# Optimization experiments

Measured on AMD Instinct MI355X. Metric: run time of the kernel, lower is better.

Reference implementation:

```python
import jax, jax.numpy as jnp
import numpy as np

SEQ = 4096
D = 1024


def setup_inputs() -> dict:
    key = jax.random.key(0)
    kx, kq, kk, kv = jax.random.split(key, 4)
    x = jax.random.normal(kx, (SEQ, D), dtype=jnp.float32)
    W_Q = jax.random.normal(kq, (D, D), dtype=jnp.float32)
    W_K = jax.random.normal(kk, (D, D), dtype=jnp.float32)
    W_V = jax.random.normal(kv, (D, D), dtype=jnp.float32)
    b_Q = jnp.zeros((D,), dtype=jnp.float32)
    b_K = jnp.zeros((D,), dtype=jnp.float32)
    b_V = jnp.zeros((D,), dtype=jnp.float32)
    return {"x": x, "W_Q": W_Q, "W_K": W_K, "W_V": W_V,
            "b_Q": b_Q, "b_K": b_K, "b_V": b_V}


def reference(x, W_Q, W_K, W_V, b_Q, b_K, b_V):
    d_head = W_Q.shape[0]
    q = x @ W_Q + b_Q                      # [S, D]
    k = x @ W_K + b_K                      # [S, D]
    v = x @ W_V + b_V                      # [S, D]
    scores = (q @ k.T) / jnp.sqrt(jnp.float32(d_head))  # [S, S]
    probs = jax.nn.softmax(scores, axis=-1)              # softmax over last axis
    return probs @ v                        # [S, D]
```

## Files before the change

kernel.cpp:

```cpp
#include <hip/hip_runtime.h>
#include <hip/hip_bf16.h>
#include <stdint.h>

#define SEQLEN 4096
#define DMODEL 1024

typedef uint16_t u16;
typedef uint32_t u32;

typedef __bf16 bf16x8 __attribute__((ext_vector_type(8)));
typedef float  f32x4  __attribute__((ext_vector_type(4)));
typedef u16    u16x8  __attribute__((ext_vector_type(8)));
typedef u16    u16x4  __attribute__((ext_vector_type(4)));

__device__ __forceinline__ u16 f2bf(float f) {
  union { float f; u32 u; } a; a.f = f;
  return (u16)((a.u + 0x7FFFu + ((a.u >> 16) & 1u)) >> 16);
}
__device__ __forceinline__ float bf2f(u16 h) {
  union { u32 u; float f; } a; a.u = ((u32)h) << 16;
  return a.f;
}

__device__ __forceinline__ void gl_lds16(const u16* g, u16* l) {
  __builtin_amdgcn_global_load_lds(
      (const __attribute__((address_space(1))) void*)g,
      (__attribute__((address_space(3))) void*)l,
      16, 0, 0);
}

__device__ __forceinline__ void stage_tile(const u16* __restrict__ g, int ld,
                                           int row0, int k0, u16* lds, int tid) {
#pragma unroll
  for (int it = 0; it < 4; ++it) {
    int u = tid + 256 * it;
    int row = u >> 3;
    int cg = (u & 7) ^ (row & 7);
    gl_lds16(g + (size_t)(row0 + row) * ld + (size_t)(k0 + cg * 8), lds + u * 8);
  }
}

__device__ __forceinline__ bf16x8 ld_frag(const u16* lds, int row, int chunk) {
  return *(const bf16x8*)(lds + row * 64 + ((chunk ^ (row & 7)) << 3));
}

#define MFMA16(c, a, b) c = __builtin_amdgcn_mfma_f32_16x16x32_bf16(a, b, c, 0, 0, 0)

__global__ void split_x_kernel(const float* __restrict__ x,
                               u16* __restrict__ xh, u16* __restrict__ xl) {
  const int total = SEQLEN * DMODEL / 4;
  for (int idx = blockIdx.x * 256 + threadIdx.x; idx < total; idx += gridDim.x * 256) {
    float4 f = ((const float4*)x)[idx];
    float ff[4] = {f.x, f.y, f.z, f.w};
    union { u16x4 v; u16 s[4]; } h, l;
#pragma unroll
    for (int uu = 0; uu < 4; ++uu) {
      u16 hi = f2bf(ff[uu]);
      h.s[uu] = hi;
      l.s[uu] = f2bf(ff[uu] - bf2f(hi));
    }
    ((u16x4*)xh)[idx] = h.v;
    ((u16x4*)xl)[idx] = l.v;
  }
}

__global__ void transpose_w_kernel(const float* __restrict__ W,
                                   u16* __restrict__ wth, u16* __restrict__ wtl) {
  __shared__ float tile[64][65];
  int n0 = (blockIdx.x & 15) * 64;
  int k0 = (blockIdx.x >> 4) * 64;
  int c = threadIdx.x & 63, r0 = threadIdx.x >> 6;
#pragma unroll
  for (int rr = 0; rr < 16; ++rr) {
    int r = r0 * 16 + rr;
    tile[r][c] = W[(size_t)(k0 + r) * DMODEL + n0 + c];
  }
  __syncthreads();
#pragma unroll
  for (int rr = 0; rr < 16; ++rr) {
    int n = r0 * 16 + rr;
    float f = tile[c][n];
    u16 hi = f2bf(f);
    wth[(size_t)(n0 + n) * DMODEL + k0 + c] = hi;
    wtl[(size_t)(n0 + n) * DMODEL + k0 + c] = f2bf(f - bf2f(hi));
  }
}

template <bool THREE, bool SPLITOUT>
__global__ __launch_bounds__(256, 2) void proj_kernel(
    const u16* __restrict__ Ah, const u16* __restrict__ Al,
    const u16* __restrict__ Bh, const u16* __restrict__ Bl,
    const float* __restrict__ bias, float scale,
    u16* __restrict__ outh, u16* __restrict__ outl, u16* __restrict__ outT) {
  __shared__ __align__(16) u16 sAh[128 * 64];
  __shared__ __align__(16) u16 sBh[128 * 64];
  __shared__ __align__(16) u16 sAl[THREE ? 128 * 64 : 8];
  __shared__ __align__(16) u16 sBl[THREE ? 128 * 64 : 8];

  int tid = threadIdx.x;
  int lane = tid & 63, wid = tid >> 6;
  int wr = (wid >> 1) * 64, wc = (wid & 1) * 64;
  int r = lane & 15, g = lane >> 4;
  int m0 = blockIdx.x * 128, n0 = blockIdx.y * 128;

  f32x4 acc[4][4];
#pragma unroll
  for (int i = 0; i < 4; ++i)
#pragma unroll
    for (int j = 0; j < 4; ++j) acc[i][j] = (f32x4){0.f, 0.f, 0.f, 0.f};

  for (int step = 0; step < DMODEL / 64; ++step) {
    int k0 = step * 64;
    __syncthreads();
    stage_tile(Ah, DMODEL, m0, k0, sAh, tid);
    stage_tile(Bh, DMODEL, n0, k0, sBh, tid);
    if (THREE) {
      stage_tile(Al, DMODEL, m0, k0, sAl, tid);
      stage_tile(Bl, DMODEL, n0, k0, sBl, tid);
    }
    __syncthreads();
#pragma unroll
    for (int ks = 0; ks < 2; ++ks) {
      bf16x8 fa[4], fb[4], fal[4], fbl[4];
#pragma unroll
      for (int i = 0; i < 4; ++i) {
        fa[i] = ld_frag(sAh, wr + i * 16 + r, ks * 4 + g);
        fb[i] = ld_frag(sBh, wc + i * 16 + r, ks * 4 + g);
      }
      if (THREE) {
#pragma unroll
        for (int i = 0; i < 4; ++i) {
          fal[i] = ld_frag(sAl, wr + i * 16 + r, ks * 4 + g);
          fbl[i] = ld_frag(sBl, wc + i * 16 + r, ks * 4 + g);
        }
      }
#pragma unroll
      for (int i = 0; i < 4; ++i)
#pragma unroll
        for (int j = 0; j < 4; ++j) {
          MFMA16(acc[i][j], fa[i], fb[j]);
          if (THREE) {
            MFMA16(acc[i][j], fa[i], fbl[j]);
            MFMA16(acc[i][j], fal[i], fb[j]);
          }
        }
    }
  }
#pragma unroll
  for (int i = 0; i < 4; ++i)
#pragma unroll
    for (int j = 0; j < 4; ++j) {
      int col = n0 + wc + j * 16 + r;
      float bv = bias[col];
#pragma unroll
      for (int t = 0; t < 4; ++t) {
        int row = m0 + wr + i * 16 + g * 4 + t;
        float v = (acc[i][j][t] + bv) * scale;
        if (SPLITOUT) {
          u16 hi = f2bf(v);
          outh[(size_t)row * DMODEL + col] = hi;
          outl[(size_t)row * DMODEL + col] = f2bf(v - bf2f(hi));
        } else {
          outT[(size_t)col * SEQLEN + row] = f2bf(v);
        }
      }
    }
}

__global__ __launch_bounds__(256, 2) void scores_kernel(
    const u16* __restrict__ qh, const u16* __restrict__ ql,
    const u16* __restrict__ kh, const u16* __restrict__ kl,
    u16* __restrict__ P, float* __restrict__ mloc, float* __restrict__ tsum) {
  __shared__ __align__(16) float sS[128 * 129];
  u16* sAh = (u16*)sS;
  u16* sAl = sAh + 128 * 64;
  u16* sBh = sAl + 128 * 64;
  u16* sBl = sBh + 128 * 64;

  int tid = threadIdx.x;
  int lane = tid & 63, wid = tid >> 6;
  int wr = (wid >> 1) * 64, wc = (wid & 1) * 64;
  int r = lane & 15, g = lane >> 4;
  int m0 = blockIdx.x * 128, n0 = blockIdx.y * 128;

  f32x4 acc[4][4];
#pragma unroll
  for (int i = 0; i < 4; ++i)
#pragma unroll
    for (int j = 0; j < 4; ++j) acc[i][j] = (f32x4){0.f, 0.f, 0.f, 0.f};

  for (int step = 0; step < DMODEL / 64; ++step) {
    int k0 = step * 64;
    __syncthreads();
    stage_tile(qh, DMODEL, m0, k0, sAh, tid);
    stage_tile(kh, DMODEL, n0, k0, sBh, tid);
    stage_tile(ql, DMODEL, m0, k0, sAl, tid);
    stage_tile(kl, DMODEL, n0, k0, sBl, tid);
    __syncthreads();
#pragma unroll
    for (int ks = 0; ks < 2; ++ks) {
      bf16x8 fa[4], fb[4], fal[4], fbl[4];
#pragma unroll
      for (int i = 0; i < 4; ++i) {
        fa[i] = ld_frag(sAh, wr + i * 16 + r, ks * 4 + g);
        fb[i] = ld_frag(sBh, wc + i * 16 + r, ks * 4 + g);
        fal[i] = ld_frag(sAl, wr + i * 16 + r, ks * 4 + g);
        fbl[i] = ld_frag(sBl, wc + i * 16 + r, ks * 4 + g);
      }
#pragma unroll
      for (int i = 0; i < 4; ++i)
#pragma unroll
        for (int j = 0; j < 4; ++j) {
          MFMA16(acc[i][j], fa[i], fb[j]);
          MFMA16(acc[i][j], fa[i], fbl[j]);
          MFMA16(acc[i][j], fal[i], fb[j]);
        }
    }
  }
  __syncthreads();
#pragma unroll
  for (int i = 0; i < 4; ++i)
#pragma unroll
    for (int j = 0; j < 4; ++j)
#pragma unroll
      for (int t = 0; t < 4; ++t)
        sS[(wr + i * 16 + g * 4 + t) * 129 + wc + j * 16 + r] = acc[i][j][t];
  __syncthreads();

  int rt = tid >> 1, h = tid & 1;
  const float* rowp = sS + rt * 129 + h * 64;
  float mx = -3.0e38f;
#pragma unroll 16
  for (int c = 0; c < 64; ++c) mx = fmaxf(mx, rowp[c]);
  mx = fmaxf(mx, __shfl_xor(mx, 1));

  float ssum = 0.f;
  int grow = m0 + rt;
  u16* pout = P + (size_t)grow * SEQLEN + n0 + h * 64;
#pragma unroll
  for (int c8 = 0; c8 < 8; ++c8) {
    union { u16 s[8]; u16x8 v; } tmp;
#pragma unroll
    for (int uu = 0; uu < 8; ++uu) {
      float e = exp2f((rowp[c8 * 8 + uu] - mx) * 1.4426950408889634f);
      ssum += e;
      tmp.s[uu] = f2bf(e);
    }
    *(u16x8*)(pout + c8 * 8) = tmp.v;
  }
  ssum += __shfl_xor(ssum, 1);
  if (h == 0) {
    mloc[(size_t)blockIdx.y * SEQLEN + grow] = mx;
    tsum[(size_t)blockIdx.y * SEQLEN + grow] = ssum;
  }
}

__global__ void finalize_kernel(const float* __restrict__ mloc,
                                const float* __restrict__ tsum,
                                float* __restrict__ rowscale) {
  int rr = blockIdx.x * 256 + threadIdx.x;
  if (rr >= SEQLEN) return;
  float M = -3.0e38f;
#pragma unroll
  for (int t = 0; t < 32; ++t) M = fmaxf(M, mloc[t * SEQLEN + rr]);
  float l = 0.f;
#pragma unroll
  for (int t = 0; t < 32; ++t)
    l += tsum[t * SEQLEN + rr] * exp2f((mloc[t * SEQLEN + rr] - M) * 1.4426950408889634f);
  float inv = 1.0f / l;
#pragma unroll
  for (int t = 0; t < 32; ++t)
    rowscale[t * SEQLEN + rr] = exp2f((mloc[t * SEQLEN + rr] - M) * 1.4426950408889634f) * inv;
}

__global__ void pnorm_kernel(u16* __restrict__ P, const float* __restrict__ rowscale) {
  const int total = SEQLEN * SEQLEN / 8;
  for (int idx = blockIdx.x * 256 + threadIdx.x; idx < total; idx += gridDim.x * 256) {
    int rrow = idx >> 9;
    int c8 = idx & 511;
    int t = c8 >> 4;
    float sc = rowscale[t * SEQLEN + rrow];
    union { u16x8 v; u16 s[8]; } d;
    d.v = ((u16x8*)P)[idx];
#pragma unroll
    for (int uu = 0; uu < 8; ++uu) d.s[uu] = f2bf(bf2f(d.s[uu]) * sc);
    ((u16x8*)P)[idx] = d.v;
  }
}

__global__ __launch_bounds__(256, 2) void pv_kernel(const u16* __restrict__ P,
                                                    const u16* __restrict__ vT,
                                                    float* __restrict__ out) {
  __shared__ __align__(16) u16 sA[128 * 64];
  __shared__ __align__(16) u16 sB[128 * 64];
  int tid = threadIdx.x;
  int lane = tid & 63, wid = tid >> 6;
  int wr = (wid >> 1) * 64, wc = (wid & 1) * 64;
  int r = lane & 15, g = lane >> 4;
  int m0 = blockIdx.x * 128, n0 = blockIdx.y * 128;

  f32x4 acc[4][4];
#pragma unroll
  for (int i = 0; i < 4; ++i)
#pragma unroll
    for (int j = 0; j < 4; ++j) acc[i][j] = (f32x4){0.f, 0.f, 0.f, 0.f};

  for (int step = 0; step < SEQLEN / 64; ++step) {
    int k0 = step * 64;
    __syncthreads();
    stage_tile(P, SEQLEN, m0, k0, sA, tid);
    stage_tile(vT, SEQLEN, n0, k0, sB, tid);
    __syncthreads();
#pragma unroll
    for (int ks = 0; ks < 2; ++ks) {
      bf16x8 fa[4], fb[4];
#pragma unroll
      for (int i = 0; i < 4; ++i) {
        fa[i] = ld_frag(sA, wr + i * 16 + r, ks * 4 + g);
        fb[i] = ld_frag(sB, wc + i * 16 + r, ks * 4 + g);
      }
#pragma unroll
      for (int i = 0; i < 4; ++i)
#pragma unroll
        for (int j = 0; j < 4; ++j) MFMA16(acc[i][j], fa[i], fb[j]);
    }
  }
#pragma unroll
  for (int i = 0; i < 4; ++i)
#pragma unroll
    for (int j = 0; j < 4; ++j)
#pragma unroll
      for (int t = 0; t < 4; ++t)
        out[(size_t)(m0 + wr + i * 16 + g * 4 + t) * DMODEL + n0 + wc + j * 16 + r] =
            acc[i][j][t];
}

extern "C" void kernel_launch(void* const* d_in, const int* in_sizes, int n_in,
                              void* d_out, int out_size, void* d_ws, size_t ws_size,
                              hipStream_t stream) {
  (void)in_sizes; (void)n_in; (void)out_size; (void)ws_size;
  const float* x  = (const float*)d_in[0];
  const float* WQ = (const float*)d_in[1];
  const float* WK = (const float*)d_in[2];
  const float* WV = (const float*)d_in[3];
  const float* bQ = (const float*)d_in[4];
  const float* bK = (const float*)d_in[5];
  const float* bV = (const float*)d_in[6];
  float* out = (float*)d_out;
  char* ws = (char*)d_ws;
  const size_t MB = 1ull << 20;

  u16* xh   = (u16*)(ws + 0);
  u16* xl   = (u16*)(ws + 8 * MB);
  u16* wqh  = (u16*)(ws + 16 * MB);
  u16* wql  = (u16*)(ws + 18 * MB);
  u16* wkh  = (u16*)(ws + 20 * MB);
  u16* wkl  = (u16*)(ws + 22 * MB);
  u16* wvh  = (u16*)(ws + 24 * MB);
  u16* wvl  = (u16*)(ws + 26 * MB);
  u16* P    = (u16*)(ws + 0);
  u16* qh   = (u16*)(ws + 32 * MB);
  u16* ql   = (u16*)(ws + 40 * MB);
  u16* kh   = (u16*)(ws + 48 * MB);
  u16* kl   = (u16*)(ws + 56 * MB);
  u16* vT   = (u16*)(ws + 64 * MB);
  float* mloc     = (float*)(ws + 72 * MB);
  float* tsum     = (float*)(ws + 72 * MB + 512 * 1024);
  float* rowscale = (float*)(ws + 73 * MB);

  split_x_kernel<<<2048, 256, 0, stream>>>(x, xh, xl);
  transpose_w_kernel<<<256, 256, 0, stream>>>(WQ, wqh, wql);
  transpose_w_kernel<<<256, 256, 0, stream>>>(WK, wkh, wkl);
  transpose_w_kernel<<<256, 256, 0, stream>>>(WV, wvh, wvl);

  dim3 gproj(32, 8);
  proj_kernel<true, true><<<gproj, 256, 0, stream>>>(xh, xl, wqh, wql, bQ,
                                                     1.0f / 32.0f, qh, ql, nullptr);
  proj_kernel<true, true><<<gproj, 256, 0, stream>>>(xh, xl, wkh, wkl, bK,
                                                     1.0f, kh, kl, nullptr);
  proj_kernel<false, false><<<gproj, 256, 0, stream>>>(xh, nullptr, wvh, nullptr, bV,
                                                       1.0f, nullptr, nullptr, vT);

  dim3 gsc(32, 32);
  scores_kernel<<<gsc, 256, 0, stream>>>(qh, ql, kh, kl, P, mloc, tsum);
  finalize_kernel<<<16, 256, 0, stream>>>(mloc, tsum, rowscale);
  pnorm_kernel<<<4096, 256, 0, stream>>>(P, rowscale);

  dim3 gpv(32, 8);
  pv_kernel<<<gpv, 256, 0, stream>>>(P, vT, out);
}
```

Baseline: 341.4 us.

## Fuse prep kernels, fold row scaling into PV, shrink LDS tiles, register softmax

Merges the x-split and three weight-transpose kernels into one launch. Removes the separate P normalization pass by applying per-tile row scales inside the PV GEMM. The three-term GEMMs now use 32-wide K tiles so LDS drops to 32KB and launch bounds allow more blocks per CU. The scores softmax works directly on accumulator registers with shuffles instead of spilling the score tile to LDS. In exchange there are twice as many K-loop barriers, extra scaling work in PV, and P is stored as scattered 2-byte writes.

```diff
diff --git a/kernel.cpp b/kernel.cpp
--- a/kernel.cpp
+++ b/kernel.cpp
@@ -29,8 +29,8 @@
       16, 0, 0);
 }
 
-__device__ __forceinline__ void stage_tile(const u16* __restrict__ g, int ld,
-                                           int row0, int k0, u16* lds, int tid) {
+__device__ __forceinline__ void stage64(const u16* __restrict__ g, int ld,
+                                        int row0, int k0, u16* lds, int tid) {
 #pragma unroll
   for (int it = 0; it < 4; ++it) {
     int u = tid + 256 * it;
@@ -39,63 +39,83 @@
     gl_lds16(g + (size_t)(row0 + row) * ld + (size_t)(k0 + cg * 8), lds + u * 8);
   }
 }
-
-__device__ __forceinline__ bf16x8 ld_frag(const u16* lds, int row, int chunk) {
+__device__ __forceinline__ void stage32(const u16* __restrict__ g, int ld,
+                                        int row0, int k0, u16* lds, int tid) {
+#pragma unroll
+  for (int it = 0; it < 2; ++it) {
+    int u = tid + 256 * it;
+    int row = u >> 2;
+    int cg = (u & 3) ^ ((row >> 1) & 3);
+    gl_lds16(g + (size_t)(row0 + row) * ld + (size_t)(k0 + cg * 8), lds + u * 8);
+  }
+}
+__device__ __forceinline__ bf16x8 frag64(const u16* lds, int row, int chunk) {
   return *(const bf16x8*)(lds + row * 64 + ((chunk ^ (row & 7)) << 3));
 }
+__device__ __forceinline__ bf16x8 frag32(const u16* lds, int row, int chunk) {
+  return *(const bf16x8*)(lds + row * 32 + ((chunk ^ ((row >> 1) & 3)) << 3));
+}
 
 #define MFMA16(c, a, b) c = __builtin_amdgcn_mfma_f32_16x16x32_bf16(a, b, c, 0, 0, 0)
 
-__global__ void split_x_kernel(const float* __restrict__ x,
-                               u16* __restrict__ xh, u16* __restrict__ xl) {
-  const int total = SEQLEN * DMODEL / 4;
-  for (int idx = blockIdx.x * 256 + threadIdx.x; idx < total; idx += gridDim.x * 256) {
-    float4 f = ((const float4*)x)[idx];
-    float ff[4] = {f.x, f.y, f.z, f.w};
-    union { u16x4 v; u16 s[4]; } h, l;
-#pragma unroll
-    for (int uu = 0; uu < 4; ++uu) {
-      u16 hi = f2bf(ff[uu]);
-      h.s[uu] = hi;
-      l.s[uu] = f2bf(ff[uu] - bf2f(hi));
-    }
-    ((u16x4*)xh)[idx] = h.v;
-    ((u16x4*)xl)[idx] = l.v;
-  }
-}
-
-__global__ void transpose_w_kernel(const float* __restrict__ W,
-                                   u16* __restrict__ wth, u16* __restrict__ wtl) {
+__global__ void prep_kernel(const float* __restrict__ x,
+                            const float* __restrict__ WQ,
+                            const float* __restrict__ WK,
+                            const float* __restrict__ WV,
+                            u16* __restrict__ xh, u16* __restrict__ xl,
+                            u16* __restrict__ wqh, u16* __restrict__ wql,
+                            u16* __restrict__ wkh, u16* __restrict__ wkl,
+                            u16* __restrict__ wvh, u16* __restrict__ wvl) {
   __shared__ float tile[64][65];
-  int n0 = (blockIdx.x & 15) * 64;
-  int k0 = (blockIdx.x >> 4) * 64;
-  int c = threadIdx.x & 63, r0 = threadIdx.x >> 6;
-#pragma unroll
-  for (int rr = 0; rr < 16; ++rr) {
-    int r = r0 * 16 + rr;
-    tile[r][c] = W[(size_t)(k0 + r) * DMODEL + n0 + c];
-  }
-  __syncthreads();
-#pragma unroll
-  for (int rr = 0; rr < 16; ++rr) {
-    int n = r0 * 16 + rr;
-    float f = tile[c][n];
-    u16 hi = f2bf(f);
-    wth[(size_t)(n0 + n) * DMODEL + k0 + c] = hi;
-    wtl[(size_t)(n0 + n) * DMODEL + k0 + c] = f2bf(f - bf2f(hi));
+  int bx = blockIdx.x;
+  if (bx < 768) {
+    const float* W = (bx < 256) ? WQ : (bx < 512) ? WK : WV;
+    u16* wth = (bx < 256) ? wqh : (bx < 512) ? wkh : wvh;
+    u16* wtl = (bx < 256) ? wql : (bx < 512) ? wkl : wvl;
+    int b = bx & 255;
+    int n0 = (b & 15) * 64;
+    int k0 = (b >> 4) * 64;
+    int c = threadIdx.x & 63, r0 = threadIdx.x >> 6;
+#pragma unroll
+    for (int rr = 0; rr < 16; ++rr) {
+      int r = r0 * 16 + rr;
+      tile[r][c] = W[(size_t)(k0 + r) * DMODEL + n0 + c];
+    }
+    __syncthreads();
+#pragma unroll
+    for (int rr = 0; rr < 16; ++rr) {
+      int n = r0 * 16 + rr;
+      float f = tile[c][n];
+      u16 hi = f2bf(f);
+      wth[(size_t)(n0 + n) * DMODEL + k0 + c] = hi;
+      wtl[(size_t)(n0 + n) * DMODEL + k0 + c] = f2bf(f - bf2f(hi));
+    }
+  } else {
+    const int total = SEQLEN * DMODEL / 4;
+    for (int idx = (bx - 768) * 256 + threadIdx.x; idx < total;
+         idx += (gridDim.x - 768) * 256) {
+      float4 f = ((const float4*)x)[idx];
+      float ff[4] = {f.x, f.y, f.z, f.w};
+      union { u16x4 v; u16 s[4]; } h, l;
+#pragma unroll
+      for (int uu = 0; uu < 4; ++uu) {
+        u16 hi = f2bf(ff[uu]);
+        h.s[uu] = hi;
+        l.s[uu] = f2bf(ff[uu] - bf2f(hi));
+      }
+      ((u16x4*)xh)[idx] = h.v;
+      ((u16x4*)xl)[idx] = l.v;
+    }
   }
 }
 
 template <bool THREE, bool SPLITOUT>
-__global__ __launch_bounds__(256, 2) void proj_kernel(
+__global__ __launch_bounds__(256, 4) void proj_kernel(
     const u16* __restrict__ Ah, const u16* __restrict__ Al,
     const u16* __restrict__ Bh, const u16* __restrict__ Bl,
     const float* __restrict__ bias, float scale,
     u16* __restrict__ outh, u16* __restrict__ outl, u16* __restrict__ outT) {
-  __shared__ __align__(16) u16 sAh[128 * 64];
-  __shared__ __align__(16) u16 sBh[128 * 64];
-  __shared__ __align__(16) u16 sAl[THREE ? 128 * 64 : 8];
-  __shared__ __align__(16) u16 sBl[THREE ? 128 * 64 : 8];
+  __shared__ __align__(16) u16 st[16384];
 
   int tid = threadIdx.x;
   int lane = tid & 63, wid = tid >> 6;
@@ -109,43 +129,55 @@
 #pragma unroll
     for (int j = 0; j < 4; ++j) acc[i][j] = (f32x4){0.f, 0.f, 0.f, 0.f};
 
-  for (int step = 0; step < DMODEL / 64; ++step) {
-    int k0 = step * 64;
-    __syncthreads();
-    stage_tile(Ah, DMODEL, m0, k0, sAh, tid);
-    stage_tile(Bh, DMODEL, n0, k0, sBh, tid);
-    if (THREE) {
-      stage_tile(Al, DMODEL, m0, k0, sAl, tid);
-      stage_tile(Bl, DMODEL, n0, k0, sBl, tid);
-    }
-    __syncthreads();
-#pragma unroll
-    for (int ks = 0; ks < 2; ++ks) {
+  if (THREE) {
+    for (int t = 0; t < DMODEL / 32; ++t) {
+      int k0 = t * 32;
+      __syncthreads();
+      stage32(Ah, DMODEL, m0, k0, st + 0 * 4096, tid);
+      stage32(Al, DMODEL, m0, k0, st + 1 * 4096, tid);
+      stage32(Bh, DMODEL, n0, k0, st + 2 * 4096, tid);
+      stage32(Bl, DMODEL, n0, k0, st + 3 * 4096, tid);
+      __syncthreads();
       bf16x8 fa[4], fb[4], fal[4], fbl[4];
 #pragma unroll
       for (int i = 0; i < 4; ++i) {
-        fa[i] = ld_frag(sAh, wr + i * 16 + r, ks * 4 + g);
-        fb[i] = ld_frag(sBh, wc + i * 16 + r, ks * 4 + g);
-      }
-      if (THREE) {
-#pragma unroll
-        for (int i = 0; i < 4; ++i) {
-          fal[i] = ld_frag(sAl, wr + i * 16 + r, ks * 4 + g);
-          fbl[i] = ld_frag(sBl, wc + i * 16 + r, ks * 4 + g);
-        }
+        fa[i]  = frag32(st + 0 * 4096, wr + i * 16 + r, g);
+        fal[i] = frag32(st + 1 * 4096, wr + i * 16 + r, g);
+        fb[i]  = frag32(st + 2 * 4096, wc + i * 16 + r, g);
+        fbl[i] = frag32(st + 3 * 4096, wc + i * 16 + r, g);
       }
 #pragma unroll
       for (int i = 0; i < 4; ++i)
 #pragma unroll
         for (int j = 0; j < 4; ++j) {
           MFMA16(acc[i][j], fa[i], fb[j]);
-          if (THREE) {
-            MFMA16(acc[i][j], fa[i], fbl[j]);
-            MFMA16(acc[i][j], fal[i], fb[j]);
-          }
+          MFMA16(acc[i][j], fa[i], fbl[j]);
+          MFMA16(acc[i][j], fal[i], fb[j]);
         }
     }
-  }
+  } else {
+    for (int t = 0; t < DMODEL / 64; ++t) {
+      int k0 = t * 64;
+      __syncthreads();
+      stage64(Ah, DMODEL, m0, k0, st + 0 * 8192, tid);
+      stage64(Bh, DMODEL, n0, k0, st + 1 * 8192, tid);
+      __syncthreads();
+#pragma unroll
+      for (int ks = 0; ks < 2; ++ks) {
+        bf16x8 fa[4], fb[4];
+#pragma unroll
+        for (int i = 0; i < 4; ++i) {
+          fa[i] = frag64(st + 0 * 8192, wr + i * 16 + r, ks * 4 + g);
+          fb[i] = frag64(st + 1 * 8192, wc + i * 16 + r, ks * 4 + g);
+        }
+#pragma unroll
+        for (int i = 0; i < 4; ++i)
+#pragma unroll
+          for (int j = 0; j < 4; ++j) MFMA16(acc[i][j], fa[i], fb[j]);
+      }
+    }
+  }
+
 #pragma unroll
   for (int i = 0; i < 4; ++i)
 #pragma unroll
@@ -167,20 +199,19 @@
     }
 }
 
-__global__ __launch_bounds__(256, 2) void scores_kernel(
+__global__ __launch_bounds__(256, 4) void scores_kernel(
     const u16* __restrict__ qh, const u16* __restrict__ ql,
     const u16* __restrict__ kh, const u16* __restrict__ kl,
     u16* __restrict__ P, float* __restrict__ mloc, float* __restrict__ tsum) {
-  __shared__ __align__(16) float sS[128 * 129];
-  u16* sAh = (u16*)sS;
-  u16* sAl = sAh + 128 * 64;
-  u16* sBh = sAl + 128 * 64;
-  u16* sBl = sBh + 128 * 64;
+  __shared__ __align__(16) u16 st[16384];
+  float* sm_max = (float*)st;
+  float* sm_sum = (float*)st + 256;
 
   int tid = threadIdx.x;
   int lane = tid & 63, wid = tid >> 6;
   int wr = (wid >> 1) * 64, wc = (wid & 1) * 64;
   int r = lane & 15, g = lane >> 4;
+  int halfid = wid & 1;
   int m0 = blockIdx.x * 128, n0 = blockIdx.y * 128;
 
   f32x4 acc[4][4];
@@ -189,69 +220,81 @@
 #pragma unroll
     for (int j = 0; j < 4; ++j) acc[i][j] = (f32x4){0.f, 0.f, 0.f, 0.f};
 
-  for (int step = 0; step < DMODEL / 64; ++step) {
-    int k0 = step * 64;
+  for (int t = 0; t < DMODEL / 32; ++t) {
+    int k0 = t * 32;
     __syncthreads();
-    stage_tile(qh, DMODEL, m0, k0, sAh, tid);
-    stage_tile(kh, DMODEL, n0, k0, sBh, tid);
-    stage_tile(ql, DMODEL, m0, k0, sAl, tid);
-    stage_tile(kl, DMODEL, n0, k0, sBl, tid);
+    stage32(qh, DMODEL, m0, k0, st + 0 * 4096, tid);
+    stage32(ql, DMODEL, m0, k0, st + 1 * 4096, tid);
+    stage32(kh, DMODEL, n0, k0, st + 2 * 4096, tid);
+    stage32(kl, DMODEL, n0, k0, st + 3 * 4096, tid);
     __syncthreads();
-#pragma unroll
-    for (int ks = 0; ks < 2; ++ks) {
-      bf16x8 fa[4], fb[4], fal[4], fbl[4];
-#pragma unroll
-      for (int i = 0; i < 4; ++i) {
-        fa[i] = ld_frag(sAh, wr + i * 16 + r, ks * 4 + g);
-        fb[i] = ld_frag(sBh, wc + i * 16 + r, ks * 4 + g);
-        fal[i] = ld_frag(sAl, wr + i * 16 + r, ks * 4 + g);
-        fbl[i] = ld_frag(sBl, wc + i * 16 + r, ks * 4 + g);
-      }
-#pragma unroll
-      for (int i = 0; i < 4; ++i)
-#pragma unroll
-        for (int j = 0; j < 4; ++j) {
-          MFMA16(acc[i][j], fa[i], fb[j]);
-          MFMA16(acc[i][j], fa[i], fbl[j]);
-          MFMA16(acc[i][j], fal[i], fb[j]);
-        }
-    }
-  }
+    bf16x8 fa[4], fb[4], fal[4], fbl[4];
+#pragma unroll
+    for (int i = 0; i < 4; ++i) {
+      fa[i]  = frag32(st + 0 * 4096, wr + i * 16 + r, g);
+      fal[i] = frag32(st + 1 * 4096, wr + i * 16 + r, g);
+      fb[i]  = frag32(st + 2 * 4096, wc + i * 16 + r, g);
+      fbl[i] = frag32(st + 3 * 4096, wc + i * 16 + r, g);
+    }
+#pragma unroll
+    for (int i = 0; i < 4; ++i)
+#pragma unroll
+      for (int j = 0; j < 4; ++j) {
+        MFMA16(acc[i][j], fa[i], fb[j]);
+        MFMA16(acc[i][j], fa[i], fbl[j]);
+        MFMA16(acc[i][j], fal[i], fb[j]);
+      }
+  }
+
   __syncthreads();
-#pragma unroll
-  for (int i = 0; i < 4; ++i)
-#pragma unroll
-    for (int j = 0; j < 4; ++j)
-#pragma unroll
-      for (int t = 0; t < 4; ++t)
-        sS[(wr + i * 16 + g * 4 + t) * 129 + wc + j * 16 + r] = acc[i][j][t];
+
+#pragma unroll
+  for (int i = 0; i < 4; ++i)
+#pragma unroll
+    for (int t = 0; t < 4; ++t) {
+      float m = fmaxf(fmaxf(acc[i][0][t], acc[i][1][t]),
+                      fmaxf(acc[i][2][t], acc[i][3][t]));
+      m = fmaxf(m, __shfl_xor(m, 1));
+      m = fmaxf(m, __shfl_xor(m, 2));
+      m = fmaxf(m, __shfl_xor(m, 4));
+      m = fmaxf(m, __shfl_xor(m, 8));
+      if (r == 0) sm_max[halfid * 128 + wr + i * 16 + g * 4 + t] = m;
+    }
   __syncthreads();
 
-  int rt = tid >> 1, h = tid & 1;
-  const float* rowp = sS + rt * 129 + h * 64;
-  float mx = -3.0e38f;
-#pragma unroll 16
-  for (int c = 0; c < 64; ++c) mx = fmaxf(mx, rowp[c]);
-  mx = fmaxf(mx, __shfl_xor(mx, 1));
-
-  float ssum = 0.f;
-  int grow = m0 + rt;
-  u16* pout = P + (size_t)grow * SEQLEN + n0 + h * 64;
-#pragma unroll
-  for (int c8 = 0; c8 < 8; ++c8) {
-    union { u16 s[8]; u16x8 v; } tmp;
-#pragma unroll
-    for (int uu = 0; uu < 8; ++uu) {
-      float e = exp2f((rowp[c8 * 8 + uu] - mx) * 1.4426950408889634f);
-      ssum += e;
-      tmp.s[uu] = f2bf(e);
-    }
-    *(u16x8*)(pout + c8 * 8) = tmp.v;
-  }
-  ssum += __shfl_xor(ssum, 1);
-  if (h == 0) {
-    mloc[(size_t)blockIdx.y * SEQLEN + grow] = mx;
-    tsum[(size_t)blockIdx.y * SEQLEN + grow] = ssum;
+#pragma unroll
+  for (int i = 0; i < 4; ++i)
+#pragma unroll
+    for (int t = 0; t < 4; ++t) {
+      int R = wr + i * 16 + g * 4 + t;
+      float mx = fmaxf(sm_max[R], sm_max[128 + R]);
+      u16* pout = P + (size_t)(m0 + R) * SEQLEN + n0 + wc + r;
+      float lsum = 0.f;
+#pragma unroll
+      for (int j = 0; j < 4; ++j) {
+        float e = exp2f((acc[i][j][t] - mx) * 1.4426950408889634f);
+        lsum += e;
+        pout[j * 16] = f2bf(e);
+      }
+      lsum += __shfl_xor(lsum, 1);
+      lsum += __shfl_xor(lsum, 2);
+      lsum += __shfl_xor(lsum, 4);
+      lsum += __shfl_xor(lsum, 8);
+      if (r == 0) sm_sum[halfid * 128 + R] = lsum;
+    }
+  __syncthreads();
+
+  if (halfid == 0 && r == 0) {
+#pragma unroll
+    for (int i = 0; i < 4; ++i)
+#pragma unroll
+      for (int t = 0; t < 4; ++t) {
+        int R = wr + i * 16 + g * 4 + t;
+        int grow = m0 + R;
+        mloc[(size_t)blockIdx.y * SEQLEN + grow] =
+            fmaxf(sm_max[R], sm_max[128 + R]);
+        tsum[(size_t)blockIdx.y * SEQLEN + grow] = sm_sum[R] + sm_sum[128 + R];
+      }
   }
 }
 
@@ -273,26 +316,10 @@
     rowscale[t * SEQLEN + rr] = exp2f((mloc[t * SEQLEN + rr] - M) * 1.4426950408889634f) * inv;
 }
 
-__global__ void pnorm_kernel(u16* __restrict__ P, const float* __restrict__ rowscale) {
-  const int total = SEQLEN * SEQLEN / 8;
-  for (int idx = blockIdx.x * 256 + threadIdx.x; idx < total; idx += gridDim.x * 256) {
-    int rrow = idx >> 9;
-    int c8 = idx & 511;
-    int t = c8 >> 4;
-    float sc = rowscale[t * SEQLEN + rrow];
-    union { u16x8 v; u16 s[8]; } d;
-    d.v = ((u16x8*)P)[idx];
-#pragma unroll
-    for (int uu = 0; uu < 8; ++uu) d.s[uu] = f2bf(bf2f(d.s[uu]) * sc);
-    ((u16x8*)P)[idx] = d.v;
-  }
-}
-
-__global__ __launch_bounds__(256, 2) void pv_kernel(const u16* __restrict__ P,
-                                                    const u16* __restrict__ vT,
-                                                    float* __restrict__ out) {
-  __shared__ __align__(16) u16 sA[128 * 64];
-  __shared__ __align__(16) u16 sB[128 * 64];
+__global__ __launch_bounds__(256, 3) void pv_kernel(
+    const u16* __restrict__ P, const u16* __restrict__ vT,
+    const float* __restrict__ rowscale, float* __restrict__ out) {
+  __shared__ __align__(16) u16 st[16384];
   int tid = threadIdx.x;
   int lane = tid & 63, wid = tid >> 6;
   int wr = (wid >> 1) * 64, wc = (wid & 1) * 64;
@@ -305,25 +332,41 @@
 #pragma unroll
     for (int j = 0; j < 4; ++j) acc[i][j] = (f32x4){0.f, 0.f, 0.f, 0.f};
 
-  for (int step = 0; step < SEQLEN / 64; ++step) {
-    int k0 = step * 64;
-    __syncthreads();
-    stage_tile(P, SEQLEN, m0, k0, sA, tid);
-    stage_tile(vT, SEQLEN, n0, k0, sB, tid);
-    __syncthreads();
-#pragma unroll
-    for (int ks = 0; ks < 2; ++ks) {
-      bf16x8 fa[4], fb[4];
-#pragma unroll
-      for (int i = 0; i < 4; ++i) {
-        fa[i] = ld_frag(sA, wr + i * 16 + r, ks * 4 + g);
-        fb[i] = ld_frag(sB, wc + i * 16 + r, ks * 4 + g);
-      }
-#pragma unroll
-      for (int i = 0; i < 4; ++i)
-#pragma unroll
-        for (int j = 0; j < 4; ++j) MFMA16(acc[i][j], fa[i], fb[j]);
-    }
+  for (int c = 0; c < SEQLEN / 128; ++c) {
+    f32x4 rs[4];
+#pragma unroll
+    for (int i = 0; i < 4; ++i)
+      rs[i] = *(const f32x4*)&rowscale[(size_t)c * SEQLEN + m0 + wr + i * 16 + g * 4];
+    f32x4 part[4][4];
+#pragma unroll
+    for (int i = 0; i < 4; ++i)
+#pragma unroll
+      for (int j = 0; j < 4; ++j) part[i][j] = (f32x4){0.f, 0.f, 0.f, 0.f};
+#pragma unroll
+    for (int s2 = 0; s2 < 2; ++s2) {
+      int k0 = c * 128 + s2 * 64;
+      __syncthreads();
+      stage64(P, SEQLEN, m0, k0, st + 0 * 8192, tid);
+      stage64(vT, SEQLEN, n0, k0, st + 1 * 8192, tid);
+      __syncthreads();
+#pragma unroll
+      for (int ks = 0; ks < 2; ++ks) {
+        bf16x8 fa[4], fb[4];
+#pragma unroll
+        for (int i = 0; i < 4; ++i) {
+          fa[i] = frag64(st + 0 * 8192, wr + i * 16 + r, ks * 4 + g);
+          fb[i] = frag64(st + 1 * 8192, wc + i * 16 + r, ks * 4 + g);
+        }
+#pragma unroll
+        for (int i = 0; i < 4; ++i)
+#pragma unroll
+          for (int j = 0; j < 4; ++j) MFMA16(part[i][j], fa[i], fb[j]);
+      }
+    }
+#pragma unroll
+    for (int i = 0; i < 4; ++i)
+#pragma unroll
+      for (int j = 0; j < 4; ++j) part[i][j] = part[i][j] * rs[i], acc[i][j] += part[i][j];
   }
 #pragma unroll
   for (int i = 0; i < 4; ++i)
@@ -368,10 +411,8 @@
   float* tsum     = (float*)(ws + 72 * MB + 512 * 1024);
   float* rowscale = (float*)(ws + 73 * MB);
 
-  split_x_kernel<<<2048, 256, 0, stream>>>(x, xh, xl);
-  transpose_w_kernel<<<256, 256, 0, stream>>>(WQ, wqh, wql);
-  transpose_w_kernel<<<256, 256, 0, stream>>>(WK, wkh, wkl);
-  transpose_w_kernel<<<256, 256, 0, stream>>>(WV, wvh, wvl);
+  prep_kernel<<<2816, 256, 0, stream>>>(x, WQ, WK, WV, xh, xl, wqh, wql,
+                                        wkh, wkl, wvh, wvl);
 
   dim3 gproj(32, 8);
   proj_kernel<true, true><<<gproj, 256, 0, stream>>>(xh, xl, wqh, wql, bQ,
@@ -384,8 +425,7 @@
   dim3 gsc(32, 32);
   scores_kernel<<<gsc, 256, 0, stream>>>(qh, ql, kh, kl, P, mloc, tsum);
   finalize_kernel<<<16, 256, 0, stream>>>(mloc, tsum, rowscale);
-  pnorm_kernel<<<4096, 256, 0, stream>>>(P, rowscale);
 
   dim3 gpv(32, 8);
-  pv_kernel<<<gpv, 256, 0, stream>>>(P, vT, out);
-}
+  pv_kernel<<<gpv, 256, 0, stream>>>(P, vT, rowscale, out);
+}
```

New measurement: 482.2 us. +41.2%, slower.
